# Kernel tuning notes

Hardware: AMD Instinct MI355X
Metric: run time of the kernel (lower is better)

## Reference

```python
import jax, jax.numpy as jnp
import numpy as np

NEG_INF = -9e15  # matches the source's -9000000000000000.0 mask fill
ALPHA = 0.2      # leaky_relu negative slope


def setup_inputs() -> dict:
    key = jax.random.key(0)
    k1, k2, k3, k4 = jax.random.split(key, 4)
    B, N, C_IN, C_OUT, H = 2, 2048, 128, 128, 16
    c = C_OUT // H  # 8 per-head features; equals H//2 so source's a-slice is consistent
    node_feats = jax.random.normal(k1, (B, N, C_IN), dtype=jnp.float32)
    # random 0/1 adjacency with self-loops
    adj = jax.random.randint(k2, (B, N, N), 0, 2).astype(jnp.float32)
    adj = jnp.maximum(adj, jnp.eye(N, dtype=jnp.float32)[None])
    # glorot-uniform-ish params
    W = jax.random.normal(k3, (C_IN, H * c), dtype=jnp.float32) * np.sqrt(2.0 / (C_IN + H * c))
    b = jnp.zeros((H * c,), dtype=jnp.float32)
    a = jax.random.normal(k4, (H, 2 * c), dtype=jnp.float32) * np.sqrt(2.0 / (H + 2 * c))
    return {"node_feats": node_feats, "adj_matrix": adj, "W": W, "b": b, "a": a}


def reference(node_feats, adj_matrix, W, b, a):
    B, N = node_feats.shape[:2]
    H = a.shape[0]
    c = a.shape[1] // 2
    # projection + split into heads: [B, N, H, c]
    h = (node_feats @ W + b).reshape(B, N, H, c)
    # additive attention halves (source slices a along last axis)
    logit_parent = jnp.einsum('bnhc,hc->bnh', h, a[:, :c])
    logit_child = jnp.einsum('bnhc,hc->bnh', h, a[:, c:])
    # dense broadcast-add logits: [B, N(i), N(j), H]
    attn_logits = logit_parent[:, :, None, :] + logit_child[:, None, :, :]
    attn_logits = jax.nn.leaky_relu(attn_logits, negative_slope=ALPHA)
    attn_logits = jnp.where(adj_matrix[..., None] == 1.0, attn_logits, NEG_INF)
    attn_probs = jax.nn.softmax(attn_logits, axis=2)  # over source nodes j
    out = jnp.einsum('bijh,bjhc->bihc', attn_probs, h)
    out = out.reshape(B, N, H * c)  # concat_heads=True
    return out, adj_matrix
```

## Files before the change

### kernel.cpp

```cpp
#include <hip/hip_runtime.h>
#include <hip/hip_bf16.h>


#define B_   2
#define N_   2048
#define CIN_ 128
#define H_   16

typedef _Float16 h2  __attribute__((ext_vector_type(2)));
typedef _Float16 v8h __attribute__((ext_vector_type(8)));
typedef float    v4f __attribute__((ext_vector_type(4)));

#define SC6 0.015625f

__device__ inline h2 pk_f16(float a, float b) {
  return __builtin_bit_cast(h2, __builtin_amdgcn_cvt_pkrtz(a, b));
}
__device__ inline unsigned as_u32(h2 v) { return __builtin_bit_cast(unsigned, v); }
__device__ inline h2 as_h2(unsigned u) { return __builtin_bit_cast(h2, u); }

__global__ __launch_bounds__(128) void proj_kernel(
    const float* __restrict__ nf, const float* __restrict__ W,
    const float* __restrict__ bias, const float* __restrict__ a,
    unsigned* __restrict__ hQ, unsigned* __restrict__ qI,
    float* __restrict__ lpT, unsigned* __restrict__ ones) {
  const int row0 = blockIdx.x * 8;
  const int t    = threadIdx.x;
  if (blockIdx.x == 0) {
    ones[t] = 0x3C003C00u; ones[t + 128] = 0x3C003C00u;
    ones[t + 256] = 0x3C003C00u; ones[t + 384] = 0x3C003C00u;
  }
  __shared__ float sNf[8][CIN_];
  {
    const float4* src = (const float4*)(nf + (long)row0 * CIN_);
    float4* dst = (float4*)(&sNf[0][0]);
    dst[t]       = src[t];
    dst[t + 128] = src[t + 128];
  }
  __syncthreads();
  float acc[8];
  const float bv = bias[t];
#pragma unroll
  for (int r = 0; r < 8; ++r) acc[r] = bv;
#pragma unroll 8
  for (int k = 0; k < CIN_; ++k) {
    const float w = W[k * 128 + t];
#pragma unroll
    for (int r = 0; r < 8; ++r) acc[r] = fmaf(sNf[r][k], w, acc[r]);
  }
  const int h = t >> 3, kc = t & 7;
  const int b = row0 >> 11, n0 = row0 & (N_ - 1);
  const int bh = b * H_ + h;
  const int cdw = n0 >> 1;
  uint4 hv;
  hv.x = as_u32(pk_f16(acc[0], acc[1]));
  hv.y = as_u32(pk_f16(acc[2], acc[3]));
  hv.z = as_u32(pk_f16(acc[4], acc[5]));
  hv.w = as_u32(pk_f16(acc[6], acc[7]));
  *(uint4*)(hQ + ((long)(bh * 8 + kc)) * (N_ / 2) + cdw) = hv;

  const float ap = a[h * 16 + kc], ac = a[h * 16 + 8 + kc];
  float lpv[8], lcv[8];
#pragma unroll
  for (int r = 0; r < 8; ++r) {
    float x = acc[r] * ap, y = acc[r] * ac;
#pragma unroll
    for (int s = 1; s < 8; s <<= 1) {
      x += __shfl_xor(x, s);
      y += __shfl_xor(y, s);
    }
    lpv[r] = x; lcv[r] = y;
  }
  if (kc == 0) {
    float4 l0 = {lpv[0], lpv[1], lpv[2], lpv[3]};
    float4 l1 = {lpv[4], lpv[5], lpv[6], lpv[7]};
    *(float4*)(lpT + (long)bh * N_ + n0)     = l0;
    *(float4*)(lpT + (long)bh * N_ + n0 + 4) = l1;
    uint4 q1, q2;
    q1.x = as_u32(pk_f16(__expf(lcv[0]) * SC6, __expf(lcv[1]) * SC6));
    q1.y = as_u32(pk_f16(__expf(lcv[2]) * SC6, __expf(lcv[3]) * SC6));
    q1.z = as_u32(pk_f16(__expf(lcv[4]) * SC6, __expf(lcv[5]) * SC6));
    q1.w = as_u32(pk_f16(__expf(lcv[6]) * SC6, __expf(lcv[7]) * SC6));
    q2.x = as_u32(pk_f16(__expf(0.2f * lcv[0]) * SC6, __expf(0.2f * lcv[1]) * SC6));
    q2.y = as_u32(pk_f16(__expf(0.2f * lcv[2]) * SC6, __expf(0.2f * lcv[3]) * SC6));
    q2.z = as_u32(pk_f16(__expf(0.2f * lcv[4]) * SC6, __expf(0.2f * lcv[5]) * SC6));
    q2.w = as_u32(pk_f16(__expf(0.2f * lcv[6]) * SC6, __expf(0.2f * lcv[7]) * SC6));
    const int addr = bh * 2048 + (cdw >> 4) * 32 + ((cdw >> 2) & 3) * 8;
    *(uint4*)(qI + addr)     = q1;
    *(uint4*)(qI + addr + 4) = q2;
  }
}

__global__ __launch_bounds__(512) void attn_kernel(
    const float* __restrict__ adj, const unsigned* __restrict__ hQ,
    const unsigned* __restrict__ qI, const float* __restrict__ lpT,
    const unsigned* __restrict__ ones, float* __restrict__ pA,
    float* __restrict__ pL, float* __restrict__ adj_out) {
  const int jh     = blockIdx.x & 1;
  const int hgroup = (blockIdx.x >> 1) & 1;
  const int rest   = blockIdx.x >> 2;
  const int b      = rest >> 7;
  const int i0     = (rest & 127) * 16;
  const int tid    = threadIdx.x;
  const int w      = tid >> 6;
  const int lane   = tid & 63;

  __shared__ uint4 sA[2048];

  {
    const long aoff = (long)(b * N_ + i0) * N_ + jh * 1024;
    const float* abase = adj + aoff;
    float* obase = adj_out + aoff;
#pragma unroll
    for (int s = 0; s < 4; ++s) {
      const int D = s * 512 + tid;
      const int mm = D & 15, qc = D >> 4;
      const int cc = (qc >> 2) * 32 + (qc & 3) * 8;
      const float4 fa = *(const float4*)(abase + mm * N_ + cc);
      const float4 fb = *(const float4*)(abase + mm * N_ + cc + 4);
      uint4 u;
      u.x = as_u32(pk_f16(fa.x, fa.y)); u.y = as_u32(pk_f16(fa.z, fa.w));
      u.z = as_u32(pk_f16(fb.x, fb.y)); u.w = as_u32(pk_f16(fb.z, fb.w));
      sA[D] = u;
      if (hgroup == 0) {
        *(float4*)(obase + mm * N_ + cc)     = fa;
        *(float4*)(obase + mm * N_ + cc + 4) = fb;
      }
    }
  }
  __syncthreads();

  const int hw = hgroup * 8 + w;
  const int bh = b * H_ + hw;
  const int m  = lane & 15;
  const int q  = lane >> 4;

  const float lp = lpT[(long)bh * N_ + i0 + m];
  const float p1 = __expf(lp) * SC6, p2 = __expf(0.2f * lp) * SC6;
  const h2 P1 = pk_f16(p1, p1), P2 = pk_f16(p2, p2);

  const unsigned* qp = qI + bh * 2048 + jh * 1024 + q * 8;
  const unsigned* hp = (m < 8) ? hQ + ((long)(bh * 8 + m)) * (N_ / 2) + jh * 512 + q * 4
                               : ones + q * 4;

  v4f acc = {0.0f, 0.0f, 0.0f, 0.0f};

  uint4 q1A = *(const uint4*)(qp),      q2A = *(const uint4*)(qp + 4),
        hA  = *(const uint4*)(hp);
  uint4 q1B = *(const uint4*)(qp + 32), q2B = *(const uint4*)(qp + 36),
        hB  = *(const uint4*)(hp + 16);

  for (int t2 = 0; t2 < 16; ++t2) {
    const int ch0 = 2 * t2, ch1 = 2 * t2 + 1;
    const int pq0 = ((ch0 + 2) & 31) * 32, ph0 = ((ch0 + 2) & 31) * 16;
    const int pq1 = ((ch1 + 2) & 31) * 32, ph1 = ((ch1 + 2) & 31) * 16;

    const uint4 q1n0 = *(const uint4*)(qp + pq0);
    const uint4 q2n0 = *(const uint4*)(qp + pq0 + 4);
    const uint4 hn0  = *(const uint4*)(hp + ph0);
    {
      const uint4 Av = sA[ch0 * 64 + lane];
      const h2 e0 = __builtin_elementwise_max(P1 * as_h2(q1A.x), P2 * as_h2(q2A.x)) * as_h2(Av.x);
      const h2 e1 = __builtin_elementwise_max(P1 * as_h2(q1A.y), P2 * as_h2(q2A.y)) * as_h2(Av.y);
      const h2 e2 = __builtin_elementwise_max(P1 * as_h2(q1A.z), P2 * as_h2(q2A.z)) * as_h2(Av.z);
      const h2 e3 = __builtin_elementwise_max(P1 * as_h2(q1A.w), P2 * as_h2(q2A.w)) * as_h2(Av.w);
      const v8h af = __builtin_bit_cast(v8h,
          (uint4){as_u32(e0), as_u32(e1), as_u32(e2), as_u32(e3)});
      acc = __builtin_amdgcn_mfma_f32_16x16x32_f16(
          af, __builtin_bit_cast(v8h, hA), acc, 0, 0, 0);
    }
    q1A = q1n0; q2A = q2n0; hA = hn0;

    const uint4 q1n1 = *(const uint4*)(qp + pq1);
    const uint4 q2n1 = *(const uint4*)(qp + pq1 + 4);
    const uint4 hn1  = *(const uint4*)(hp + ph1);
    {
      const uint4 Av = sA[ch1 * 64 + lane];
      const h2 e0 = __builtin_elementwise_max(P1 * as_h2(q1B.x), P2 * as_h2(q2B.x)) * as_h2(Av.x);
      const h2 e1 = __builtin_elementwise_max(P1 * as_h2(q1B.y), P2 * as_h2(q2B.y)) * as_h2(Av.y);
      const h2 e2 = __builtin_elementwise_max(P1 * as_h2(q1B.z), P2 * as_h2(q2B.z)) * as_h2(Av.z);
      const h2 e3 = __builtin_elementwise_max(P1 * as_h2(q1B.w), P2 * as_h2(q2B.w)) * as_h2(Av.w);
      const v8h af = __builtin_bit_cast(v8h,
          (uint4){as_u32(e0), as_u32(e1), as_u32(e2), as_u32(e3)});
      acc = __builtin_amdgcn_mfma_f32_16x16x32_f16(
          af, __builtin_bit_cast(v8h, hB), acc, 0, 0, 0);
    }
    q1B = q1n1; q2B = q2n1; hB = hn1;
  }

#pragma unroll
  for (int r = 0; r < 4; ++r) {
    const int gidx = (b * N_ + i0 + q * 4 + r) * H_ + hw;
    if (m < 8)   pA[(long)jh * 524288 + (long)gidx * 8 + m] = acc[r];
    if (m == 8)  pL[jh * 65536 + gidx] = acc[r];
  }
}

__global__ __launch_bounds__(512) void combine_kernel(
    const float* __restrict__ pA, const float* __restrict__ pL,
    float* __restrict__ out) {
  const int g = blockIdx.x * 512 + threadIdx.x;
  const float s = pL[g >> 3] + pL[(g >> 3) + 65536];
  const float v = pA[g] + pA[g + 524288];
  out[g] = v / s;
}

extern "C" void kernel_launch(void* const* d_in, const int* in_sizes, int n_in,
                              void* d_out, int out_size, void* d_ws, size_t ws_size,
                              hipStream_t stream) {
  const float* nf   = (const float*)d_in[0];
  const float* adj  = (const float*)d_in[1];
  const float* W    = (const float*)d_in[2];
  const float* bias = (const float*)d_in[3];
  const float* a    = (const float*)d_in[4];

  float* out     = (float*)d_out;
  float* adj_out = out + (long)B_ * N_ * H_ * 8;

  unsigned* ws   = (unsigned*)d_ws;
  unsigned* hQ   = ws;
  unsigned* qI   = ws + 262144;
  float*    lpT  = (float*)(ws + 327680);
  unsigned* ones = ws + 393216;
  float*    pA   = (float*)(ws + 393728);
  float*    pL   = (float*)(ws + 1442304);

  hipLaunchKernelGGL(proj_kernel, dim3(B_ * N_ / 8), dim3(128), 0, stream,
                     nf, W, bias, a, hQ, qI, lpT, ones);
  hipLaunchKernelGGL(attn_kernel, dim3(B_ * (N_ / 16) * 2 * 2), dim3(512), 0,
                     stream, adj, hQ, qI, lpT, ones, pA, pL, adj_out);
  hipLaunchKernelGGL(combine_kernel, dim3(1024), dim3(512), 0, stream,
                     pA, pL, out);
}
```

Before: 144.6 us.

## Process 32 query rows per block and split source nodes four ways

The attention kernel now handles two 16-row tiles of query nodes per block, so each loaded qI/hQ chunk feeds two MFMAs. The source dimension is split into four quarters instead of two, which keeps the block count unchanged and needs four partial sums in the combine kernel. The projection kernel moves to 4 rows per block and writes packed outputs at half width. The aim is to cut global loads of the per-column factors and values per unit of work. The cost is more partial-sum traffic in the workspace and more register pressure from two accumulators.

```diff
diff --git a/kernel.cpp b/kernel.cpp
--- a/kernel.cpp
+++ b/kernel.cpp
@@ -24,45 +24,38 @@
     const float* __restrict__ bias, const float* __restrict__ a,
     unsigned* __restrict__ hQ, unsigned* __restrict__ qI,
     float* __restrict__ lpT, unsigned* __restrict__ ones) {
-  const int row0 = blockIdx.x * 8;
+  const int row0 = blockIdx.x * 4;
   const int t    = threadIdx.x;
   if (blockIdx.x == 0) {
     ones[t] = 0x3C003C00u; ones[t + 128] = 0x3C003C00u;
     ones[t + 256] = 0x3C003C00u; ones[t + 384] = 0x3C003C00u;
   }
-  __shared__ float sNf[8][CIN_];
-  {
-    const float4* src = (const float4*)(nf + (long)row0 * CIN_);
-    float4* dst = (float4*)(&sNf[0][0]);
-    dst[t]       = src[t];
-    dst[t + 128] = src[t + 128];
-  }
+  __shared__ float sNf[4][CIN_];
+  ((float4*)&sNf[0][0])[t] = ((const float4*)(nf + (long)row0 * CIN_))[t];
   __syncthreads();
-  float acc[8];
+  float acc[4];
   const float bv = bias[t];
 #pragma unroll
-  for (int r = 0; r < 8; ++r) acc[r] = bv;
+  for (int r = 0; r < 4; ++r) acc[r] = bv;
 #pragma unroll 8
   for (int k = 0; k < CIN_; ++k) {
     const float w = W[k * 128 + t];
 #pragma unroll
-    for (int r = 0; r < 8; ++r) acc[r] = fmaf(sNf[r][k], w, acc[r]);
+    for (int r = 0; r < 4; ++r) acc[r] = fmaf(sNf[r][k], w, acc[r]);
   }
   const int h = t >> 3, kc = t & 7;
   const int b = row0 >> 11, n0 = row0 & (N_ - 1);
   const int bh = b * H_ + h;
   const int cdw = n0 >> 1;
-  uint4 hv;
+  uint2 hv;
   hv.x = as_u32(pk_f16(acc[0], acc[1]));
   hv.y = as_u32(pk_f16(acc[2], acc[3]));
-  hv.z = as_u32(pk_f16(acc[4], acc[5]));
-  hv.w = as_u32(pk_f16(acc[6], acc[7]));
-  *(uint4*)(hQ + ((long)(bh * 8 + kc)) * (N_ / 2) + cdw) = hv;
+  *(uint2*)(hQ + ((long)(bh * 8 + kc)) * (N_ / 2) + cdw) = hv;
 
   const float ap = a[h * 16 + kc], ac = a[h * 16 + 8 + kc];
-  float lpv[8], lcv[8];
-#pragma unroll
-  for (int r = 0; r < 8; ++r) {
+  float lpv[4], lcv[4];
+#pragma unroll
+  for (int r = 0; r < 4; ++r) {
     float x = acc[r] * ap, y = acc[r] * ac;
 #pragma unroll
     for (int s = 1; s < 8; s <<= 1) {
@@ -73,21 +66,16 @@
   }
   if (kc == 0) {
     float4 l0 = {lpv[0], lpv[1], lpv[2], lpv[3]};
-    float4 l1 = {lpv[4], lpv[5], lpv[6], lpv[7]};
-    *(float4*)(lpT + (long)bh * N_ + n0)     = l0;
-    *(float4*)(lpT + (long)bh * N_ + n0 + 4) = l1;
-    uint4 q1, q2;
+    *(float4*)(lpT + (long)bh * N_ + n0) = l0;
+    uint2 q1, q2;
     q1.x = as_u32(pk_f16(__expf(lcv[0]) * SC6, __expf(lcv[1]) * SC6));
     q1.y = as_u32(pk_f16(__expf(lcv[2]) * SC6, __expf(lcv[3]) * SC6));
-    q1.z = as_u32(pk_f16(__expf(lcv[4]) * SC6, __expf(lcv[5]) * SC6));
-    q1.w = as_u32(pk_f16(__expf(lcv[6]) * SC6, __expf(lcv[7]) * SC6));
     q2.x = as_u32(pk_f16(__expf(0.2f * lcv[0]) * SC6, __expf(0.2f * lcv[1]) * SC6));
     q2.y = as_u32(pk_f16(__expf(0.2f * lcv[2]) * SC6, __expf(0.2f * lcv[3]) * SC6));
-    q2.z = as_u32(pk_f16(__expf(0.2f * lcv[4]) * SC6, __expf(0.2f * lcv[5]) * SC6));
-    q2.w = as_u32(pk_f16(__expf(0.2f * lcv[6]) * SC6, __expf(0.2f * lcv[7]) * SC6));
     const int addr = bh * 2048 + (cdw >> 4) * 32 + ((cdw >> 2) & 3) * 8;
-    *(uint4*)(qI + addr)     = q1;
-    *(uint4*)(qI + addr + 4) = q2;
+    const int off  = cdw & 3;
+    *(uint2*)(qI + addr + off)     = q1;
+    *(uint2*)(qI + addr + 4 + off) = q2;
   }
 }
 
@@ -96,11 +84,11 @@
     const unsigned* __restrict__ qI, const float* __restrict__ lpT,
     const unsigned* __restrict__ ones, float* __restrict__ pA,
     float* __restrict__ pL, float* __restrict__ adj_out) {
-  const int jh     = blockIdx.x & 1;
-  const int hgroup = (blockIdx.x >> 1) & 1;
-  const int rest   = blockIdx.x >> 2;
-  const int b      = rest >> 7;
-  const int i0     = (rest & 127) * 16;
+  const int jq     = blockIdx.x & 3;
+  const int hgroup = (blockIdx.x >> 2) & 1;
+  const int rest   = blockIdx.x >> 3;
+  const int b      = rest >> 6;
+  const int i0     = (rest & 63) * 32;
   const int tid    = threadIdx.x;
   const int w      = tid >> 6;
   const int lane   = tid & 63;
@@ -108,23 +96,25 @@
   __shared__ uint4 sA[2048];
 
   {
-    const long aoff = (long)(b * N_ + i0) * N_ + jh * 1024;
+    const long aoff = (long)(b * N_ + i0) * N_ + jq * 512;
     const float* abase = adj + aoff;
     float* obase = adj_out + aoff;
 #pragma unroll
     for (int s = 0; s < 4; ++s) {
       const int D = s * 512 + tid;
-      const int mm = D & 15, qc = D >> 4;
+      const int u = D >> 10, loc = D & 1023;
+      const int mm = loc & 15, qc = loc >> 4;
       const int cc = (qc >> 2) * 32 + (qc & 3) * 8;
-      const float4 fa = *(const float4*)(abase + mm * N_ + cc);
-      const float4 fb = *(const float4*)(abase + mm * N_ + cc + 4);
-      uint4 u;
-      u.x = as_u32(pk_f16(fa.x, fa.y)); u.y = as_u32(pk_f16(fa.z, fa.w));
-      u.z = as_u32(pk_f16(fb.x, fb.y)); u.w = as_u32(pk_f16(fb.z, fb.w));
-      sA[D] = u;
+      const int row = u * 16 + mm;
+      const float4 fa = *(const float4*)(abase + (long)row * N_ + cc);
+      const float4 fb = *(const float4*)(abase + (long)row * N_ + cc + 4);
+      uint4 uu;
+      uu.x = as_u32(pk_f16(fa.x, fa.y)); uu.y = as_u32(pk_f16(fa.z, fa.w));
+      uu.z = as_u32(pk_f16(fb.x, fb.y)); uu.w = as_u32(pk_f16(fb.z, fb.w));
+      sA[D] = uu;
       if (hgroup == 0) {
-        *(float4*)(obase + mm * N_ + cc)     = fa;
-        *(float4*)(obase + mm * N_ + cc + 4) = fb;
+        *(float4*)(obase + (long)row * N_ + cc)     = fa;
+        *(float4*)(obase + (long)row * N_ + cc + 4) = fb;
       }
     }
   }
@@ -135,39 +125,54 @@
   const int m  = lane & 15;
   const int q  = lane >> 4;
 
-  const float lp = lpT[(long)bh * N_ + i0 + m];
-  const float p1 = __expf(lp) * SC6, p2 = __expf(0.2f * lp) * SC6;
-  const h2 P1 = pk_f16(p1, p1), P2 = pk_f16(p2, p2);
-
-  const unsigned* qp = qI + bh * 2048 + jh * 1024 + q * 8;
-  const unsigned* hp = (m < 8) ? hQ + ((long)(bh * 8 + m)) * (N_ / 2) + jh * 512 + q * 4
-                               : ones + q * 4;
-
-  v4f acc = {0.0f, 0.0f, 0.0f, 0.0f};
+  const float lpa = lpT[(long)bh * N_ + i0 + m];
+  const float lpb = lpT[(long)bh * N_ + i0 + 16 + m];
+  const h2 P1a = pk_f16(__expf(lpa) * SC6, __expf(lpa) * SC6);
+  const h2 P2a = pk_f16(__expf(0.2f * lpa) * SC6, __expf(0.2f * lpa) * SC6);
+  const h2 P1b = pk_f16(__expf(lpb) * SC6, __expf(lpb) * SC6);
+  const h2 P2b = pk_f16(__expf(0.2f * lpb) * SC6, __expf(0.2f * lpb) * SC6);
+
+  const unsigned* qp = qI + bh * 2048 + jq * 512 + q * 8;
+  const unsigned* hp = (m < 8)
+      ? hQ + ((long)(bh * 8 + m)) * (N_ / 2) + jq * 256 + q * 4
+      : ones + q * 4;
+
+  v4f acc0 = {0.0f, 0.0f, 0.0f, 0.0f};
+  v4f acc1 = {0.0f, 0.0f, 0.0f, 0.0f};
 
   uint4 q1A = *(const uint4*)(qp),      q2A = *(const uint4*)(qp + 4),
         hA  = *(const uint4*)(hp);
   uint4 q1B = *(const uint4*)(qp + 32), q2B = *(const uint4*)(qp + 36),
         hB  = *(const uint4*)(hp + 16);
 
-  for (int t2 = 0; t2 < 16; ++t2) {
+  for (int t2 = 0; t2 < 8; ++t2) {
     const int ch0 = 2 * t2, ch1 = 2 * t2 + 1;
-    const int pq0 = ((ch0 + 2) & 31) * 32, ph0 = ((ch0 + 2) & 31) * 16;
-    const int pq1 = ((ch1 + 2) & 31) * 32, ph1 = ((ch1 + 2) & 31) * 16;
+    const int pq0 = ((ch0 + 2) & 15) * 32, ph0 = ((ch0 + 2) & 15) * 16;
+    const int pq1 = ((ch1 + 2) & 15) * 32, ph1 = ((ch1 + 2) & 15) * 16;
 
     const uint4 q1n0 = *(const uint4*)(qp + pq0);
     const uint4 q2n0 = *(const uint4*)(qp + pq0 + 4);
     const uint4 hn0  = *(const uint4*)(hp + ph0);
     {
-      const uint4 Av = sA[ch0 * 64 + lane];
-      const h2 e0 = __builtin_elementwise_max(P1 * as_h2(q1A.x), P2 * as_h2(q2A.x)) * as_h2(Av.x);
-      const h2 e1 = __builtin_elementwise_max(P1 * as_h2(q1A.y), P2 * as_h2(q2A.y)) * as_h2(Av.y);
-      const h2 e2 = __builtin_elementwise_max(P1 * as_h2(q1A.z), P2 * as_h2(q2A.z)) * as_h2(Av.z);
-      const h2 e3 = __builtin_elementwise_max(P1 * as_h2(q1A.w), P2 * as_h2(q2A.w)) * as_h2(Av.w);
-      const v8h af = __builtin_bit_cast(v8h,
-          (uint4){as_u32(e0), as_u32(e1), as_u32(e2), as_u32(e3)});
-      acc = __builtin_amdgcn_mfma_f32_16x16x32_f16(
-          af, __builtin_bit_cast(v8h, hA), acc, 0, 0, 0);
+      const uint4 Av0 = sA[ch0 * 64 + lane];
+      const uint4 Av1 = sA[1024 + ch0 * 64 + lane];
+      const v8h bf = __builtin_bit_cast(v8h, hA);
+      const h2 Q1x = as_h2(q1A.x), Q1y = as_h2(q1A.y), Q1z = as_h2(q1A.z), Q1w = as_h2(q1A.w);
+      const h2 Q2x = as_h2(q2A.x), Q2y = as_h2(q2A.y), Q2z = as_h2(q2A.z), Q2w = as_h2(q2A.w);
+      const uint4 af0 = {
+        as_u32(__builtin_elementwise_max(P1a * Q1x, P2a * Q2x) * as_h2(Av0.x)),
+        as_u32(__builtin_elementwise_max(P1a * Q1y, P2a * Q2y) * as_h2(Av0.y)),
+        as_u32(__builtin_elementwise_max(P1a * Q1z, P2a * Q2z) * as_h2(Av0.z)),
+        as_u32(__builtin_elementwise_max(P1a * Q1w, P2a * Q2w) * as_h2(Av0.w))};
+      acc0 = __builtin_amdgcn_mfma_f32_16x16x32_f16(
+          __builtin_bit_cast(v8h, af0), bf, acc0, 0, 0, 0);
+      const uint4 af1 = {
+        as_u32(__builtin_elementwise_max(P1b * Q1x, P2b * Q2x) * as_h2(Av1.x)),
+        as_u32(__builtin_elementwise_max(P1b * Q1y, P2b * Q2y) * as_h2(Av1.y)),
+        as_u32(__builtin_elementwise_max(P1b * Q1z, P2b * Q2z) * as_h2(Av1.z)),
+        as_u32(__builtin_elementwise_max(P1b * Q1w, P2b * Q2w) * as_h2(Av1.w))};
+      acc1 = __builtin_amdgcn_mfma_f32_16x16x32_f16(
+          __builtin_bit_cast(v8h, af1), bf, acc1, 0, 0, 0);
     }
     q1A = q1n0; q2A = q2n0; hA = hn0;
 
@@ -175,24 +180,38 @@
     const uint4 q2n1 = *(const uint4*)(qp + pq1 + 4);
     const uint4 hn1  = *(const uint4*)(hp + ph1);
     {
-      const uint4 Av = sA[ch1 * 64 + lane];
-      const h2 e0 = __builtin_elementwise_max(P1 * as_h2(q1B.x), P2 * as_h2(q2B.x)) * as_h2(Av.x);
-      const h2 e1 = __builtin_elementwise_max(P1 * as_h2(q1B.y), P2 * as_h2(q2B.y)) * as_h2(Av.y);
-      const h2 e2 = __builtin_elementwise_max(P1 * as_h2(q1B.z), P2 * as_h2(q2B.z)) * as_h2(Av.z);
-      const h2 e3 = __builtin_elementwise_max(P1 * as_h2(q1B.w), P2 * as_h2(q2B.w)) * as_h2(Av.w);
-      const v8h af = __builtin_bit_cast(v8h,
-          (uint4){as_u32(e0), as_u32(e1), as_u32(e2), as_u32(e3)});
-      acc = __builtin_amdgcn_mfma_f32_16x16x32_f16(
-          af, __builtin_bit_cast(v8h, hB), acc, 0, 0, 0);
+      const uint4 Av0 = sA[ch1 * 64 + lane];
+      const uint4 Av1 = sA[1024 + ch1 * 64 + lane];
+      const v8h bf = __builtin_bit_cast(v8h, hB);
+      const h2 Q1x = as_h2(q1B.x), Q1y = as_h2(q1B.y), Q1z = as_h2(q1B.z), Q1w = as_h2(q1B.w);
+      const h2 Q2x = as_h2(q2B.x), Q2y = as_h2(q2B.y), Q2z = as_h2(q2B.z), Q2w = as_h2(q2B.w);
+      const uint4 af0 = {
+        as_u32(__builtin_elementwise_max(P1a * Q1x, P2a * Q2x) * as_h2(Av0.x)),
+        as_u32(__builtin_elementwise_max(P1a * Q1y, P2a * Q2y) * as_h2(Av0.y)),
+        as_u32(__builtin_elementwise_max(P1a * Q1z, P2a * Q2z) * as_h2(Av0.z)),
+        as_u32(__builtin_elementwise_max(P1a * Q1w, P2a * Q2w) * as_h2(Av0.w))};
+      acc0 = __builtin_amdgcn_mfma_f32_16x16x32_f16(
+          __builtin_bit_cast(v8h, af0), bf, acc0, 0, 0, 0);
+      const uint4 af1 = {
+        as_u32(__builtin_elementwise_max(P1b * Q1x, P2b * Q2x) * as_h2(Av1.x)),
+        as_u32(__builtin_elementwise_max(P1b * Q1y, P2b * Q2y) * as_h2(Av1.y)),
+        as_u32(__builtin_elementwise_max(P1b * Q1z, P2b * Q2z) * as_h2(Av1.z)),
+        as_u32(__builtin_elementwise_max(P1b * Q1w, P2b * Q2w) * as_h2(Av1.w))};
+      acc1 = __builtin_amdgcn_mfma_f32_16x16x32_f16(
+          __builtin_bit_cast(v8h, af1), bf, acc1, 0, 0, 0);
     }
     q1B = q1n1; q2B = q2n1; hB = hn1;
   }
 
 #pragma unroll
-  for (int r = 0; r < 4; ++r) {
-    const int gidx = (b * N_ + i0 + q * 4 + r) * H_ + hw;
-    if (m < 8)   pA[(long)jh * 524288 + (long)gidx * 8 + m] = acc[r];
-    if (m == 8)  pL[jh * 65536 + gidx] = acc[r];
+  for (int u = 0; u < 2; ++u) {
+    const v4f av = u ? acc1 : acc0;
+#pragma unroll
+    for (int r = 0; r < 4; ++r) {
+      const int gidx = (b * N_ + i0 + u * 16 + q * 4 + r) * H_ + hw;
+      if (m < 8)  pA[jq * 524288 + (long)gidx * 8 + m] = av[r];
+      if (m == 8) pL[jq * 65536 + gidx] = av[r];
+    }
   }
 }
 
@@ -200,8 +219,9 @@
     const float* __restrict__ pA, const float* __restrict__ pL,
     float* __restrict__ out) {
   const int g = blockIdx.x * 512 + threadIdx.x;
-  const float s = pL[g >> 3] + pL[(g >> 3) + 65536];
-  const float v = pA[g] + pA[g + 524288];
+  const int gl = g >> 3;
+  const float s = pL[gl] + pL[gl + 65536] + pL[gl + 131072] + pL[gl + 196608];
+  const float v = pA[g] + pA[g + 524288] + pA[g + 1048576] + pA[g + 1572864];
   out[g] = v / s;
 }
 
@@ -223,11 +243,11 @@
   float*    lpT  = (float*)(ws + 327680);
   unsigned* ones = ws + 393216;
   float*    pA   = (float*)(ws + 393728);
-  float*    pL   = (float*)(ws + 1442304);
-
-  hipLaunchKernelGGL(proj_kernel, dim3(B_ * N_ / 8), dim3(128), 0, stream,
+  float*    pL   = (float*)(ws + 2490880);
+
+  hipLaunchKernelGGL(proj_kernel, dim3(B_ * N_ / 4), dim3(128), 0, stream,
                      nf, W, bias, a, hQ, qI, lpT, ones);
-  hipLaunchKernelGGL(attn_kernel, dim3(B_ * (N_ / 16) * 2 * 2), dim3(512), 0,
+  hipLaunchKernelGGL(attn_kernel, dim3(B_ * (N_ / 32) * 2 * 4), dim3(512), 0,
                      stream, adj, hQ, qI, lpT, ones, pA, pL, adj_out);
   hipLaunchKernelGGL(combine_kernel, dim3(1024), dim3(512), 0, stream,
                      pA, pL, out);
```

New measurement: 131.4 us. 9.1% less time.
